# Optimization experiments

Measured on AMD Instinct MI355X. Metric: run time of the kernel, lower is better.

## Reference

```python
import jax, jax.numpy as jnp
import numpy as np

B, S, E, H = 2, 2048, 1024, 16
D = E // H  # head_dim = 64


def setup_inputs() -> dict:
    key = jax.random.key(0)
    ks = jax.random.split(key, 6)
    sc = 1.0 / np.sqrt(D)
    return {
        "x": jax.random.normal(ks[0], (B, S, E), dtype=jnp.float32),
        "Wq": jax.random.normal(ks[1], (D, D), dtype=jnp.float32) * sc,
        "Wk": jax.random.normal(ks[2], (D, D), dtype=jnp.float32) * sc,
        "Wv": jax.random.normal(ks[3], (D, D), dtype=jnp.float32) * sc,
        "Wo": jax.random.normal(ks[4], (E, E), dtype=jnp.float32) * (1.0 / np.sqrt(E)),
        "bo": jnp.zeros((E,), dtype=jnp.float32),
    }


def reference(x, Wq, Wk, Wv, Wo, bo):
    b, s, e = x.shape
    # split into heads: (B, H, S, D)
    xh = x.reshape(b, s, H, D).transpose(0, 2, 1, 3)
    # per-head linear projections (weights SHARED across heads); torch Linear: x @ W^T
    q = jnp.einsum('bhsd,ed->bhse', xh, Wq)
    k = jnp.einsum('bhsd,ed->bhse', xh, Wk)
    v = jnp.einsum('bhsd,ed->bhse', xh, Wv)
    # full attention matrix (B, H, S, S) — faithful to the naive original
    energy = jnp.einsum('bhqd,bhkd->bhqk', q, k)
    attn = jax.nn.softmax(energy / jnp.sqrt(jnp.asarray(D, x.dtype)), axis=-1)
    out = jnp.einsum('bhqk,bhkd->bhqd', attn, v)
    out = out.transpose(0, 2, 1, 3).reshape(b, s, e)
    return out @ Wo.T + bo
```

## Files before the change

kernel.cpp:

```cpp
#include <hip/hip_runtime.h>
#include <hip/hip_bf16.h>

#define B 2
#define S 2048
#define E 1024
#define H 16
#define D 64

typedef unsigned short ushort_t;
typedef __attribute__((ext_vector_type(8))) short bf16x8;
typedef __attribute__((ext_vector_type(4))) float f32x4;
typedef __attribute__((ext_vector_type(16))) float f32x16;

static __device__ __forceinline__ ushort_t f2bf(float f) {
    union { float f; unsigned u; } v; v.f = f;
    unsigned r = v.u + 0x7fffu + ((v.u >> 16) & 1u);
    return (ushort_t)(r >> 16);
}

#define MFMA(a, b, c)   __builtin_amdgcn_mfma_f32_16x16x32_bf16((a), (b), (c), 0, 0, 0)
#define MFMA32(a, b, c) __builtin_amdgcn_mfma_f32_32x32x16_bf16((a), (b), (c), 0, 0, 0)
#define PACKBF(hi, lo) __builtin_amdgcn_perm((hi), (lo), 0x07060302u)

__global__ __launch_bounds__(256) void qkv_proj(
    const float* __restrict__ x,
    const float* __restrict__ Wq, const float* __restrict__ Wk, const float* __restrict__ Wv,
    const float* __restrict__ Wo,
    ushort_t* __restrict__ q, ushort_t* __restrict__ k, ushort_t* __restrict__ vT,
    ushort_t* __restrict__ wob)
{
    __shared__ ushort_t Xs[64][72];
    __shared__ ushort_t Wqs[64][72], Wks[64][72], Wvs[64][72];
    int t = threadIdx.x;
    int bh = blockIdx.y, b = bh >> 4, h = bh & 15;
    int s0 = blockIdx.x * 64;

    {
        int woid = blockIdx.y * 32 + blockIdx.x;
        int i = woid * 1024 + t * 4;
        float4 f = *(const float4*)(Wo + i);
        ushort4 u2; u2.x = f2bf(f.x); u2.y = f2bf(f.y); u2.z = f2bf(f.z); u2.w = f2bf(f.w);
        *(ushort4*)(wob + i) = u2;
    }
    {
        int i = t >> 2, d0 = (t & 3) * 16;
        const float* xp = x + ((size_t)(b * S + s0 + i)) * E + h * D + d0;
        #pragma unroll
        for (int c = 0; c < 16; c += 4) {
            float4 f = *(const float4*)(xp + c);
            Xs[i][d0 + c + 0] = f2bf(f.x); Xs[i][d0 + c + 1] = f2bf(f.y);
            Xs[i][d0 + c + 2] = f2bf(f.z); Xs[i][d0 + c + 3] = f2bf(f.w);
        }
    }
    {
        int e = t >> 2, d0 = (t & 3) * 16;
        const float* wqp = Wq + e * 64 + d0;
        const float* wkp = Wk + e * 64 + d0;
        const float* wvp = Wv + e * 64 + d0;
        #pragma unroll
        for (int c = 0; c < 16; c += 4) {
            float4 fq = *(const float4*)(wqp + c);
            Wqs[e][d0 + c + 0] = f2bf(fq.x * 0.18033688011112042f);
            Wqs[e][d0 + c + 1] = f2bf(fq.y * 0.18033688011112042f);
            Wqs[e][d0 + c + 2] = f2bf(fq.z * 0.18033688011112042f);
            Wqs[e][d0 + c + 3] = f2bf(fq.w * 0.18033688011112042f);
            float4 fk = *(const float4*)(wkp + c);
            Wks[e][d0 + c + 0] = f2bf(fk.x); Wks[e][d0 + c + 1] = f2bf(fk.y);
            Wks[e][d0 + c + 2] = f2bf(fk.z); Wks[e][d0 + c + 3] = f2bf(fk.w);
            float4 fv = *(const float4*)(wvp + c);
            Wvs[e][d0 + c + 0] = f2bf(fv.x); Wvs[e][d0 + c + 1] = f2bf(fv.y);
            Wvs[e][d0 + c + 2] = f2bf(fv.z); Wvs[e][d0 + c + 3] = f2bf(fv.w);
        }
    }
    __syncthreads();

    int w = t >> 6, lane = t & 63, m = lane & 15, quad = lane >> 4;
    bf16x8 a0 = *(bf16x8*)&Xs[16 * w + m][quad * 8];
    bf16x8 a1 = *(bf16x8*)&Xs[16 * w + m][32 + quad * 8];
    f32x4 cq[4], ck[4], cv[4];
    #pragma unroll
    for (int nt = 0; nt < 4; nt++) { cq[nt] = (f32x4)0.f; ck[nt] = (f32x4)0.f; cv[nt] = (f32x4)0.f; }
    #pragma unroll
    for (int nt = 0; nt < 4; nt++) {
        bf16x8 b0, b1;
        b0 = *(bf16x8*)&Wqs[nt * 16 + m][quad * 8]; b1 = *(bf16x8*)&Wqs[nt * 16 + m][32 + quad * 8];
        cq[nt] = MFMA(a0, b0, cq[nt]); cq[nt] = MFMA(a1, b1, cq[nt]);
        b0 = *(bf16x8*)&Wks[nt * 16 + m][quad * 8]; b1 = *(bf16x8*)&Wks[nt * 16 + m][32 + quad * 8];
        ck[nt] = MFMA(a0, b0, ck[nt]); ck[nt] = MFMA(a1, b1, ck[nt]);
        b0 = *(bf16x8*)&Wvs[nt * 16 + m][quad * 8]; b1 = *(bf16x8*)&Wvs[nt * 16 + m][32 + quad * 8];
        cv[nt] = MFMA(a0, b0, cv[nt]); cv[nt] = MFMA(a1, b1, cv[nt]);
    }
    size_t base = (size_t)bh * S + s0;
    #pragma unroll
    for (int nt = 0; nt < 4; nt++)
        #pragma unroll
        for (int r = 0; r < 4; r++) {
            size_t idx = (base + 16 * w + quad * 4 + r) * D + nt * 16 + m;
            q[idx] = f2bf(cq[nt][r]);
            k[idx] = f2bf(ck[nt][r]);
        }
    __syncthreads();
    #pragma unroll
    for (int nt = 0; nt < 4; nt++)
        #pragma unroll
        for (int r = 0; r < 4; r++)
            Wvs[nt * 16 + m][16 * w + quad * 4 + r] = f2bf(cv[nt][r]);
    __syncthreads();
    {
        int d0 = t >> 2, sc = (t & 3) * 16;
        ushort_t* vp = vT + ((size_t)bh * D + d0) * S + s0 + sc;
        *(bf16x8*)(vp)     = *(bf16x8*)&Wvs[d0][sc];
        *(bf16x8*)(vp + 8) = *(bf16x8*)&Wvs[d0][sc + 8];
    }
}

__global__ __launch_bounds__(512, 4) void flash_attn(
    const ushort_t* __restrict__ q, const ushort_t* __restrict__ k,
    const ushort_t* __restrict__ vT, ushort_t* __restrict__ ao)
{
    __shared__ ushort_t Ks[2][2][64][72];
    __shared__ ushort_t Vt[2][2][64][72];
    int t = threadIdx.x;
    int lin = blockIdx.x;
    int xcd = lin & 7, loc = lin >> 3;
    int bh = xcd * 4 + (loc >> 4);
    int q0 = (loc & 15) * 128;
    int b = bh >> 4, h = bh & 15;
    int w = t >> 6, lane = t & 63, l31 = lane & 31, half = lane >> 5;
    int g = w >> 2, wq = w & 3;
    int tg = t & 255;

    const ushort_t* qb = q + ((size_t)bh * S + q0) * D;
    const ushort_t* kb = k + (size_t)bh * S * D;
    const ushort_t* vb = vT + (size_t)bh * D * S;

    bf16x8 qf[4];
    {
        const ushort_t* qp = qb + (size_t)(wq * 32 + l31) * D + half * 8;
        #pragma unroll
        for (int c = 0; c < 4; c++) qf[c] = *(const bf16x8*)(qp + c * 16);
    }

    f32x16 o0 = (f32x16)0.f, o1 = (f32x16)0.f;
    float2 ls2 = make_float2(0.f, 0.f);

    int sr = tg >> 2, scc = (tg & 3) * 16;
    bf16x8 kp0, kp1, vp0, vp1;

    {
        int k00 = g * 64;
        const ushort_t* kp = kb + (size_t)(k00 + sr) * D + scc;
        const ushort_t* vp = vb + (size_t)sr * S + k00 + scc;
        kp0 = *(const bf16x8*)(kp);     kp1 = *(const bf16x8*)(kp + 8);
        vp0 = *(const bf16x8*)(vp);     vp1 = *(const bf16x8*)(vp + 8);
        *(bf16x8*)&Ks[g][0][sr][scc]     = kp0;
        *(bf16x8*)&Ks[g][0][sr][scc + 8] = kp1;
        *(bf16x8*)&Vt[g][0][sr][scc]     = vp0;
        *(bf16x8*)&Vt[g][0][sr][scc + 8] = vp1;
    }
    __syncthreads();
    {
        int k01 = (2 + g) * 64;
        const ushort_t* kp = kb + (size_t)(k01 + sr) * D + scc;
        const ushort_t* vp = vb + (size_t)sr * S + k01 + scc;
        kp0 = *(const bf16x8*)(kp);     kp1 = *(const bf16x8*)(kp + 8);
        vp0 = *(const bf16x8*)(vp);     vp1 = *(const bf16x8*)(vp + 8);
    }

    const int NJ = S / 128;
    for (int jt = 0; jt < NJ; jt++) {
        int p = jt & 1;
        if (jt + 1 < NJ) {
            *(bf16x8*)&Ks[g][1 - p][sr][scc]     = kp0;
            *(bf16x8*)&Ks[g][1 - p][sr][scc + 8] = kp1;
            *(bf16x8*)&Vt[g][1 - p][sr][scc]     = vp0;
            *(bf16x8*)&Vt[g][1 - p][sr][scc + 8] = vp1;
        }
        if (jt + 2 < NJ) {
            int k0n = (2 * (jt + 2) + g) * 64;
            const ushort_t* kp = kb + (size_t)(k0n + sr) * D + scc;
            const ushort_t* vp = vb + (size_t)sr * S + k0n + scc;
            kp0 = *(const bf16x8*)(kp);     kp1 = *(const bf16x8*)(kp + 8);
            vp0 = *(const bf16x8*)(vp);     vp1 = *(const bf16x8*)(vp + 8);
        }

        union { unsigned u[4]; bf16x8 v; } pa[4];
        #pragma unroll
        for (int st = 0; st < 2; st++) {
            f32x16 e = (f32x16)0.f;
            __builtin_amdgcn_s_setprio(1);
            #pragma unroll
            for (int c = 0; c < 4; c++) {
                bf16x8 ka = *(bf16x8*)&Ks[g][p][st * 32 + l31][c * 16 + half * 8];
                e = MFMA32(ka, qf[c], e);
            }
            __builtin_amdgcn_s_setprio(0);
            unsigned pt[16];
            #pragma unroll
            for (int r = 0; r < 16; r += 2) {
                float pe0 = __builtin_amdgcn_exp2f(e[r]);
                float pe1 = __builtin_amdgcn_exp2f(e[r + 1]);
                ls2.x += pe0; ls2.y += pe1;
                pt[r]     = __float_as_uint(pe0);
                pt[r + 1] = __float_as_uint(pe1);
            }
            #pragma unroll
            for (int c2 = 0; c2 < 2; c2++) {
                int rb = c2 * 8;
                unsigned dA = PACKBF(pt[rb + 1], pt[rb + 0]);
                unsigned dB = PACKBF(pt[rb + 3], pt[rb + 2]);
                unsigned dC = PACKBF(pt[rb + 5], pt[rb + 4]);
                unsigned dD = PACKBF(pt[rb + 7], pt[rb + 6]);
                asm volatile("v_permlane32_swap_b32 %0, %1" : "+v"(dA), "+v"(dC));
                asm volatile("v_permlane32_swap_b32 %0, %1" : "+v"(dB), "+v"(dD));
                int kc = st * 2 + c2;
                pa[kc].u[0] = dA;
                pa[kc].u[1] = dB;
                pa[kc].u[2] = dC;
                pa[kc].u[3] = dD;
            }
        }

        __builtin_amdgcn_s_setprio(1);
        #pragma unroll
        for (int kc = 0; kc < 4; kc++) {
            bf16x8 vf0 = *(bf16x8*)&Vt[g][p][l31][kc * 16 + half * 8];
            bf16x8 vf1 = *(bf16x8*)&Vt[g][p][32 + l31][kc * 16 + half * 8];
            o0 = MFMA32(pa[kc].v, vf0, o0);
            o1 = MFMA32(pa[kc].v, vf1, o1);
        }
        __builtin_amdgcn_s_setprio(0);
        __syncthreads();
    }

    float lsum = ls2.x + ls2.y;
    float* cmb = (float*)&Ks[0][0][0][0];
    int slot = (wq * 64 + lane) * 33;
    if (g == 1) {
        #pragma unroll
        for (int r2 = 0; r2 < 16; r2++) { cmb[slot + r2] = o0[r2]; cmb[slot + 16 + r2] = o1[r2]; }
        cmb[slot + 32] = lsum;
    }
    __syncthreads();
    if (g == 0) {
        #pragma unroll
        for (int r2 = 0; r2 < 16; r2++) { o0[r2] += cmb[slot + r2]; o1[r2] += cmb[slot + 16 + r2]; }
        lsum += cmb[slot + 32];
        float lfull = lsum + __shfl_xor(lsum, 32, 64);
        float inv = 1.001953125f / lfull;
        #pragma unroll
        for (int reg = 0; reg < 16; reg++) {
            int qrow = (reg & 3) + 8 * (reg >> 2) + 4 * half;
            float li = __shfl(inv, qrow, 64);
            int srow = q0 + wq * 32 + qrow;
            size_t base2 = ((size_t)(b * S + srow)) * E + h * D + l31;
            ao[base2]      = f2bf(o0[reg] * li);
            ao[base2 + 32] = f2bf(o1[reg] * li);
        }
    }
}

__global__ __launch_bounds__(512) void out_proj(
    const ushort_t* __restrict__ A, const ushort_t* __restrict__ Wob,
    const float* __restrict__ bo, float* __restrict__ Y)
{
    __shared__ ushort_t As[2][128][72];
    __shared__ ushort_t Ws[2][64][72];
    int t = threadIdx.x;
    int hwb = blockIdx.x;
    int swz = (hwb & 7) * 64 + (hwb >> 3);
    int n0 = (swz & 15) * 64, m0 = (swz >> 4) * 128;
    int w = t >> 6, lane = t & 63, m = lane & 15, quad = lane >> 4;
    f32x4 acc[4];
    #pragma unroll
    for (int nt = 0; nt < 4; nt++) acc[nt] = (f32x4)0.f;

    int ar = t >> 2, ac = (t & 3) * 16;
    int wr = t >> 3, wc = (t & 7) * 8;
    const ushort_t* apb = A + (size_t)(m0 + ar) * E + ac;
    const ushort_t* wpb = Wob + (size_t)(n0 + wr) * E + wc;

    bf16x8 arg[2], wrg;
    {
        *(bf16x8*)&As[0][ar][ac]     = *(const bf16x8*)(apb);
        *(bf16x8*)&As[0][ar][ac + 8] = *(const bf16x8*)(apb + 8);
        *(bf16x8*)&Ws[0][wr][wc]     = *(const bf16x8*)(wpb);
    }
    __syncthreads();
    {
        arg[0] = *(const bf16x8*)(apb + 64);
        arg[1] = *(const bf16x8*)(apb + 64 + 8);
        wrg    = *(const bf16x8*)(wpb + 64);
    }

    const int KT = E / 64;
    for (int ks = 0; ks < KT; ks++) {
        int p = ks & 1;
        if (ks + 1 < KT) {
            *(bf16x8*)&As[1 - p][ar][ac]     = arg[0];
            *(bf16x8*)&As[1 - p][ar][ac + 8] = arg[1];
            *(bf16x8*)&Ws[1 - p][wr][wc]     = wrg;
        }
        if (ks + 2 < KT) {
            int off = (ks + 2) * 64;
            arg[0] = *(const bf16x8*)(apb + off);
            arg[1] = *(const bf16x8*)(apb + off + 8);
            wrg    = *(const bf16x8*)(wpb + off);
        }
        #pragma unroll
        for (int h2 = 0; h2 < 2; h2++) {
            bf16x8 af = *(bf16x8*)&As[p][w * 16 + m][h2 * 32 + quad * 8];
            #pragma unroll
            for (int nt = 0; nt < 4; nt++) {
                bf16x8 bfr = *(bf16x8*)&Ws[p][nt * 16 + m][h2 * 32 + quad * 8];
                acc[nt] = MFMA(af, bfr, acc[nt]);
            }
        }
        __syncthreads();
    }
    #pragma unroll
    for (int nt = 0; nt < 4; nt++)
        #pragma unroll
        for (int r = 0; r < 4; r++) {
            int row = m0 + w * 16 + quad * 4 + r;
            int col = n0 + nt * 16 + m;
            Y[(size_t)row * E + col] = acc[nt][r] + bo[col];
        }
}

extern "C" void kernel_launch(void* const* d_in, const int* in_sizes, int n_in,
                              void* d_out, int out_size, void* d_ws, size_t ws_size,
                              hipStream_t stream)
{
    const float* x  = (const float*)d_in[0];
    const float* Wq = (const float*)d_in[1];
    const float* Wk = (const float*)d_in[2];
    const float* Wv = (const float*)d_in[3];
    const float* Wo = (const float*)d_in[4];
    const float* bo = (const float*)d_in[5];
    float* Y = (float*)d_out;

    const size_t n = (size_t)B * H * S * D;
    ushort_t* qw  = (ushort_t*)d_ws;
    ushort_t* kw  = qw + n;
    ushort_t* vTw = kw + n;
    ushort_t* ao  = vTw + n;
    ushort_t* wob = ao + n;

    qkv_proj<<<dim3(S / 64, B * H), 256, 0, stream>>>(x, Wq, Wk, Wv, Wo, qw, kw, vTw, wob);
    flash_attn<<<dim3((S / 128) * B * H), 512, 0, stream>>>(qw, kw, vTw, ao);
    out_proj<<<dim3(512), 512, 0, stream>>>(ao, wob, bo, Y);
}
```

Measured before the change: 144.7 us.

## Load K/V MFMA fragments directly from global memory, drop LDS staging

Removes the double-buffered LDS staging of K and V tiles and the per-iteration barrier; each wave now reads its MFMA operands straight from global memory (relying on L1/L2), with LDS used only for the final cross-group combine. Launch bounds are raised to ask for more resident blocks. This removes LDS write/read traffic and block-wide synchronisation, but the four waves in a group now each fetch the same K/V data from cache with less coalesced access, and the global loads are no longer prefetched ahead of use, so latency may be exposed.

```diff
diff --git a/kernel.cpp b/kernel.cpp
--- a/kernel.cpp
+++ b/kernel.cpp
@@ -114,12 +114,11 @@
     }
 }
 
-__global__ __launch_bounds__(512, 4) void flash_attn(
+__global__ __launch_bounds__(512, 8) void flash_attn(
     const ushort_t* __restrict__ q, const ushort_t* __restrict__ k,
     const ushort_t* __restrict__ vT, ushort_t* __restrict__ ao)
 {
-    __shared__ ushort_t Ks[2][2][64][72];
-    __shared__ ushort_t Vt[2][2][64][72];
+    __shared__ float cmb[256 * 33];
     int t = threadIdx.x;
     int lin = blockIdx.x;
     int xcd = lin & 7, loc = lin >> 3;
@@ -128,7 +127,6 @@
     int b = bh >> 4, h = bh & 15;
     int w = t >> 6, lane = t & 63, l31 = lane & 31, half = lane >> 5;
     int g = w >> 2, wq = w & 3;
-    int tg = t & 255;
 
     const ushort_t* qb = q + ((size_t)bh * S + q0) * D;
     const ushort_t* kb = k + (size_t)bh * S * D;
@@ -141,57 +139,26 @@
         for (int c = 0; c < 4; c++) qf[c] = *(const bf16x8*)(qp + c * 16);
     }
 
+    const ushort_t* kr  = kb + (size_t)l31 * D + half * 8;
+    const ushort_t* v0r = vb + (size_t)l31 * S + half * 8;
+    const ushort_t* v1r = vb + (size_t)(32 + l31) * S + half * 8;
+
     f32x16 o0 = (f32x16)0.f, o1 = (f32x16)0.f;
     float2 ls2 = make_float2(0.f, 0.f);
 
-    int sr = tg >> 2, scc = (tg & 3) * 16;
-    bf16x8 kp0, kp1, vp0, vp1;
-
-    {
-        int k00 = g * 64;
-        const ushort_t* kp = kb + (size_t)(k00 + sr) * D + scc;
-        const ushort_t* vp = vb + (size_t)sr * S + k00 + scc;
-        kp0 = *(const bf16x8*)(kp);     kp1 = *(const bf16x8*)(kp + 8);
-        vp0 = *(const bf16x8*)(vp);     vp1 = *(const bf16x8*)(vp + 8);
-        *(bf16x8*)&Ks[g][0][sr][scc]     = kp0;
-        *(bf16x8*)&Ks[g][0][sr][scc + 8] = kp1;
-        *(bf16x8*)&Vt[g][0][sr][scc]     = vp0;
-        *(bf16x8*)&Vt[g][0][sr][scc + 8] = vp1;
-    }
-    __syncthreads();
-    {
-        int k01 = (2 + g) * 64;
-        const ushort_t* kp = kb + (size_t)(k01 + sr) * D + scc;
-        const ushort_t* vp = vb + (size_t)sr * S + k01 + scc;
-        kp0 = *(const bf16x8*)(kp);     kp1 = *(const bf16x8*)(kp + 8);
-        vp0 = *(const bf16x8*)(vp);     vp1 = *(const bf16x8*)(vp + 8);
-    }
-
     const int NJ = S / 128;
     for (int jt = 0; jt < NJ; jt++) {
-        int p = jt & 1;
-        if (jt + 1 < NJ) {
-            *(bf16x8*)&Ks[g][1 - p][sr][scc]     = kp0;
-            *(bf16x8*)&Ks[g][1 - p][sr][scc + 8] = kp1;
-            *(bf16x8*)&Vt[g][1 - p][sr][scc]     = vp0;
-            *(bf16x8*)&Vt[g][1 - p][sr][scc + 8] = vp1;
-        }
-        if (jt + 2 < NJ) {
-            int k0n = (2 * (jt + 2) + g) * 64;
-            const ushort_t* kp = kb + (size_t)(k0n + sr) * D + scc;
-            const ushort_t* vp = vb + (size_t)sr * S + k0n + scc;
-            kp0 = *(const bf16x8*)(kp);     kp1 = *(const bf16x8*)(kp + 8);
-            vp0 = *(const bf16x8*)(vp);     vp1 = *(const bf16x8*)(vp + 8);
-        }
+        int k0 = (2 * jt + g) * 64;
 
         union { unsigned u[4]; bf16x8 v; } pa[4];
         #pragma unroll
         for (int st = 0; st < 2; st++) {
             f32x16 e = (f32x16)0.f;
+            const ushort_t* kp = kr + (size_t)(k0 + st * 32) * D;
             __builtin_amdgcn_s_setprio(1);
             #pragma unroll
             for (int c = 0; c < 4; c++) {
-                bf16x8 ka = *(bf16x8*)&Ks[g][p][st * 32 + l31][c * 16 + half * 8];
+                bf16x8 ka = *(const bf16x8*)(kp + c * 16);
                 e = MFMA32(ka, qf[c], e);
             }
             __builtin_amdgcn_s_setprio(0);
@@ -224,17 +191,15 @@
         __builtin_amdgcn_s_setprio(1);
         #pragma unroll
         for (int kc = 0; kc < 4; kc++) {
-            bf16x8 vf0 = *(bf16x8*)&Vt[g][p][l31][kc * 16 + half * 8];
-            bf16x8 vf1 = *(bf16x8*)&Vt[g][p][32 + l31][kc * 16 + half * 8];
+            bf16x8 vf0 = *(const bf16x8*)(v0r + k0 + kc * 16);
+            bf16x8 vf1 = *(const bf16x8*)(v1r + k0 + kc * 16);
             o0 = MFMA32(pa[kc].v, vf0, o0);
             o1 = MFMA32(pa[kc].v, vf1, o1);
         }
         __builtin_amdgcn_s_setprio(0);
-        __syncthreads();
     }
 
     float lsum = ls2.x + ls2.y;
-    float* cmb = (float*)&Ks[0][0][0][0];
     int slot = (wq * 64 + lane) * 33;
     if (g == 1) {
         #pragma unroll
```

Measured after the change: 372.0 us. 157% more time.
